# Performance work log

Hardware: AMD Instinct MI355X
Metric: run time of the kernel (lower is better)

Reference implementation:

```python
import jax, jax.numpy as jnp
import numpy as np

H = 128        # hidden_dim
NP = 512       # program nodes
NV = 50000     # voxel nodes
E = 800000     # cross edges (16 per voxel)
TAU = 1.0
SLOPE = 0.01   # LeakyReLU default negative slope


def setup_inputs() -> dict:
    key = jax.random.key(0)
    ks = jax.random.split(key, 12)
    s = 1.0 / np.sqrt(H)
    x = jax.random.normal(ks[0], (NP, H), dtype=jnp.float32)
    v = jax.random.normal(ks[1], (NV, H), dtype=jnp.float32)
    row0 = jax.random.randint(ks[2], (E,), 0, NP, dtype=jnp.int32)
    row1 = (jnp.arange(E, dtype=jnp.int32) % NV)  # every voxel gets E/NV edges
    cross_edge_index = jnp.stack([row0, row1])    # [2, E]
    W_program = jax.random.normal(ks[3], (H, H), dtype=jnp.float32) * s
    b_program = jnp.zeros((H,), dtype=jnp.float32)
    W_voxel = jax.random.normal(ks[4], (H, H), dtype=jnp.float32) * s
    b_voxel = jnp.zeros((H,), dtype=jnp.float32)
    W_m1 = jax.random.normal(ks[5], (H, H), dtype=jnp.float32) * s
    b_m1 = jnp.zeros((H,), dtype=jnp.float32)
    W_m2 = jax.random.normal(ks[6], (H, 1), dtype=jnp.float32) * s
    b_m2 = jnp.zeros((1,), dtype=jnp.float32)
    theta = jax.random.normal(ks[7], (H, 1), dtype=jnp.float32) * s  # xavier-like
    u = jax.random.uniform(ks[8], (E,), dtype=jnp.float32)
    gumbel_u = jnp.clip(u, 1e-7, 1.0 - 1e-7)  # avoid log(0)
    return {"x": x, "v": v, "cross_edge_index": cross_edge_index,
            "W_program": W_program, "b_program": b_program,
            "W_voxel": W_voxel, "b_voxel": b_voxel,
            "W_m1": W_m1, "b_m1": b_m1, "W_m2": W_m2, "b_m2": b_m2,
            "theta": theta, "gumbel_u": gumbel_u}


def reference(x, v, cross_edge_index, W_program, b_program, W_voxel, b_voxel,
              W_m1, b_m1, W_m2, b_m2, theta, gumbel_u):
    src = cross_edge_index[0]
    dst = cross_edge_index[1]
    x_sel = x[src]                      # [E, H] gather
    v_sel = v[dst]                      # [E, H] gather
    # mask = sigmoid(MLP(v)) : Linear -> LeakyReLU -> Linear(H,1)
    a = v @ W_m1 + b_m1
    a = jnp.where(a >= 0, a, SLOPE * a)
    mask = jax.nn.sigmoid(a @ W_m2 + b_m2)                  # [NV, 1]
    # attention logits: theta^T * tanh(Wp x_sel + Wv v_sel), summed over H
    t = jnp.tanh(x_sel @ W_program + b_program + v_sel @ W_voxel + b_voxel)
    e = jnp.sum(t * theta[:, 0], axis=-1)                   # [E]
    # Gumbel softmax: global softmax over all edges (dim=0 in torch on 1-D e)
    g = -jnp.log(-jnp.log(gumbel_u))
    y = jax.nn.softmax((e + g) / TAU)                       # [E]
    # per-voxel hard argmax (scatter_max), straight-through estimator
    seg_max = jax.ops.segment_max(y, dst, num_segments=NV)  # [NV]
    is_max = y == seg_max[dst]
    cand = jnp.where(is_max, jnp.arange(E), E)
    argmax = jax.ops.segment_min(cand, dst, num_segments=NV)  # [NV], first max per voxel
    y_hard_1 = jnp.zeros(E + 1, y.dtype).at[argmax].set(1.0)[:E]  # overflow slot for empty segments
    y_hard = jax.lax.stop_gradient(y_hard_1 - y) + y
    # scatter-sum of soft-attended program features back to voxels
    summed = jax.ops.segment_sum(x_sel * y[:, None], dst, num_segments=NV)  # [NV, H]
    v_out = v + mask * summed
    return (v_out, mask, y[:, None], y_hard[:, None])
```

## Files before the change

### kernel.cpp

```cpp
#include <hip/hip_runtime.h>

#define H     128
#define NP    512
#define NVOX  50000
#define NEDGE 800000
#define EPV   16
#define SLOPE 0.01f
#define GR    32
#define NBLK  1563
#define STRH  136
#define VSTR  132
#define C1    2.8853900817779268f
#define LOG2E 1.4426950408889634f
#define ABLK  3125

#define EXP2(x) __builtin_amdgcn_exp2f(x)
#define LOG2(x) __builtin_amdgcn_logf(x)
#define RCP(x)  __builtin_amdgcn_rcpf(x)

typedef _Float16 h16;
typedef __attribute__((ext_vector_type(4))) _Float16 h16x4;
typedef __attribute__((ext_vector_type(8))) _Float16 h16x8;
typedef __attribute__((ext_vector_type(4))) float    f32x4;

template <int CTRL>
__device__ __forceinline__ float dpp_add(float x) {
    union { float f; int i; } u, r;
    u.f = x;
    r.i = __builtin_amdgcn_update_dpp(0, u.i, CTRL, 0xf, 0xf, true);
    return x + r.f;
}

__global__ __launch_bounds__(256) void k_pre(const float* __restrict__ x,
                                             const float* __restrict__ Wp,
                                             const float* __restrict__ bp,
                                             const float* __restrict__ Wv,
                                             const float* __restrict__ Wm1,
                                             float* __restrict__ xpout,
                                             h16* __restrict__ WvThi,
                                             h16* __restrict__ WvTlo,
                                             h16* __restrict__ Wm1T) {
    __shared__ float part[H];
    int bid = blockIdx.x;
    int tid = threadIdx.x;
    if (bid < NP) {
        int row = bid;
        int col = tid & 127;
        int kh  = tid >> 7;
        int kbase = kh * 64;
        const float* xr = x + (size_t)row * H;
        float acc = 0.f;
#pragma unroll 8
        for (int k = 0; k < 64; ++k)
            acc = fmaf(xr[kbase + k], Wp[(size_t)(kbase + k) * H + col], acc);
        if (kh == 1) part[col] = acc;
        __syncthreads();
        if (kh == 0) xpout[(size_t)row * H + col] = (acc + part[col] + bp[col]) * C1;
    } else {
        int idx = (bid - NP) * 256 + tid;
        if (idx < 16384) {
            int k = idx >> 7, n = idx & 127;
            float w = Wv[idx];
            h16 hi = (h16)w;
            WvThi[n * H + k] = hi;
            WvTlo[n * H + k] = (h16)(w - (float)hi);
        } else {
            int j = idx - 16384;
            int k = j >> 7, n = j & 127;
            Wm1T[n * H + k] = (h16)Wm1[j];
        }
    }
}

__global__ __launch_bounds__(256, 4) void k_mainX(
    const float* __restrict__ v,   const float* __restrict__ x,
    const float* __restrict__ bv,  const float* __restrict__ bm1,
    const float* __restrict__ Wm2, const float* __restrict__ bm2,
    const h16* __restrict__ WvThi, const h16* __restrict__ WvTlo,
    const h16* __restrict__ Wm1T,
    const float* __restrict__ xp,  const int* __restrict__ cei,
    const float* __restrict__ theta, const float* __restrict__ gum,
    float* __restrict__ mask_out, float* __restrict__ pout,
    float* __restrict__ sump,     float* __restrict__ partial)
{
    __shared__ __align__(16) char ldsbuf[2 * GR * STRH * 2];
    h16*   vh = (h16*)ldsbuf;
    h16*   vl = vh + GR * STRH;
    float* vt = (float*)ldsbuf;
    __shared__ int   ceit[EPV * GR];
    __shared__ float gumt[EPV * GR];
    __shared__ float pmbuf[4][GR];
    __shared__ float psums[4];

    int tid  = threadIdx.x;
    int base = blockIdx.x * GR;

#pragma unroll
    for (int i = 0; i < 4; ++i) {
        int f  = i * 256 + tid;
        int r  = f >> 5, c4 = f & 31;
        int gr = base + r; if (gr >= NVOX) gr = NVOX - 1;
        float4 val = *(const float4*)&v[(size_t)gr * H + c4 * 4];
        h16x4 hi, lo;
        hi.x = (h16)val.x; lo.x = (h16)(val.x - (float)hi.x);
        hi.y = (h16)val.y; lo.y = (h16)(val.y - (float)hi.y);
        hi.z = (h16)val.z; lo.z = (h16)(val.z - (float)hi.z);
        hi.w = (h16)val.w; lo.w = (h16)(val.w - (float)hi.w);
        *(h16x4*)&vh[r * STRH + c4 * 4] = hi;
        *(h16x4*)&vl[r * STRH + c4 * 4] = lo;
    }
#pragma unroll
    for (int it = 0; it < 2; ++it) {
        int idx = it * 256 + tid;
        int t = idx >> 5, c = idx & 31;
        int vx = base + c; if (vx >= NVOX) vx = NVOX - 1;
        int e = vx + t * NVOX;
        ceit[idx] = cei[e];
        gumt[idx] = -LOG2E * RCP(LOG2(gum[e]));
    }
    __syncthreads();

    int wave = tid >> 6, lane = tid & 63;
    int m16 = lane & 15, quad = lane >> 4;
    int cb = wave * 32;

    f32x4 aV[2][2], aM[2][2];
#pragma unroll
    for (int rt = 0; rt < 2; ++rt)
#pragma unroll
        for (int ct = 0; ct < 2; ++ct) { aV[rt][ct] = (f32x4)0.f; aM[rt][ct] = (f32x4)0.f; }

#pragma unroll
    for (int kc = 0; kc < 4; ++kc) {
        int kofs = kc * 32 + quad * 8;
        h16x8 ah[2], al[2];
#pragma unroll
        for (int rt = 0; rt < 2; ++rt) {
            int row = rt * 16 + m16;
            ah[rt] = *(const h16x8*)&vh[row * STRH + kofs];
            al[rt] = *(const h16x8*)&vl[row * STRH + kofs];
        }
#pragma unroll
        for (int ct = 0; ct < 2; ++ct) {
            int n = cb + ct * 16 + m16;
            h16x8 bh = *(const h16x8*)&WvThi[n * H + kofs];
            h16x8 bl = *(const h16x8*)&WvTlo[n * H + kofs];
            h16x8 bm = *(const h16x8*)&Wm1T[n * H + kofs];
#pragma unroll
            for (int rt = 0; rt < 2; ++rt) {
                aV[rt][ct] = __builtin_amdgcn_mfma_f32_16x16x32_f16(ah[rt], bh, aV[rt][ct], 0, 0, 0);
                aV[rt][ct] = __builtin_amdgcn_mfma_f32_16x16x32_f16(al[rt], bh, aV[rt][ct], 0, 0, 0);
                aV[rt][ct] = __builtin_amdgcn_mfma_f32_16x16x32_f16(ah[rt], bl, aV[rt][ct], 0, 0, 0);
                aM[rt][ct] = __builtin_amdgcn_mfma_f32_16x16x32_f16(ah[rt], bm, aM[rt][ct], 0, 0, 0);
            }
        }
    }
    __syncthreads();

    float pml[2][4];
#pragma unroll
    for (int rt = 0; rt < 2; ++rt)
#pragma unroll
        for (int reg = 0; reg < 4; ++reg) pml[rt][reg] = 0.f;
#pragma unroll
    for (int ct = 0; ct < 2; ++ct) {
        int col = cb + ct * 16 + m16;
        float bvc = bv[col], bmc = bm1[col], w2c = Wm2[col];
#pragma unroll
        for (int rt = 0; rt < 2; ++rt)
#pragma unroll
            for (int reg = 0; reg < 4; ++reg) {
                int row = rt * 16 + quad * 4 + reg;
                vt[row * VSTR + col] = (aV[rt][ct][reg] + bvc) * C1;
                float m = aM[rt][ct][reg] + bmc;
                m = (m >= 0.f) ? m : SLOPE * m;
                pml[rt][reg] = fmaf(m, w2c, pml[rt][reg]);
            }
    }
#pragma unroll
    for (int rt = 0; rt < 2; ++rt)
#pragma unroll
        for (int reg = 0; reg < 4; ++reg) {
            pml[rt][reg] = dpp_add<0xB1>(pml[rt][reg]);
            pml[rt][reg] = dpp_add<0x4E>(pml[rt][reg]);
            pml[rt][reg] = dpp_add<0x141>(pml[rt][reg]);
            pml[rt][reg] = dpp_add<0x140>(pml[rt][reg]);
        }
    if (m16 == 0) {
#pragma unroll
        for (int rt = 0; rt < 2; ++rt)
#pragma unroll
            for (int reg = 0; reg < 4; ++reg)
                pmbuf[wave][rt * 16 + quad * 4 + reg] = pml[rt][reg];
    }
    __syncthreads();
    if (wave == 0 && lane < GR) {
        int gr = base + lane;
        if (gr < NVOX) {
            float s = pmbuf[0][lane] + pmbuf[1][lane] + pmbuf[2][lane]
                    + pmbuf[3][lane] + bm2[0];
            mask_out[gr] = RCP(1.f + EXP2(-s * LOG2E));
        }
    }

    int g = tid >> 3, lk = tid & 7;
    int vox = base + g;
    bool valid = vox < NVOX;
    float th2[16], thsum = 0.f;
#pragma unroll
    for (int i = 0; i < 4; ++i) {
        float4 t4 = *(const float4*)&theta[(lk + 8 * i) * 4];
        th2[i * 4 + 0] = -2.f * LOG2E * t4.x; th2[i * 4 + 1] = -2.f * LOG2E * t4.y;
        th2[i * 4 + 2] = -2.f * LOG2E * t4.z; th2[i * 4 + 3] = -2.f * LOG2E * t4.w;
        thsum += LOG2E * (t4.x + t4.y + t4.z + t4.w);
    }
    const float* vr = &vt[g * VSTR];
    float4 b0 = *(const float4*)&vr[(lk +  0) * 4];
    float4 b1 = *(const float4*)&vr[(lk +  8) * 4];
    float4 b2 = *(const float4*)&vr[(lk + 16) * 4];
    float4 b3 = *(const float4*)&vr[(lk + 24) * 4];

    float4 s0 = make_float4(0.f,0.f,0.f,0.f), s1 = s0, s2 = s0, s3 = s0;
    float psum = 0.f, pmax = -1.f;
    int   pidx = 0;

    int srcC = ceit[g];
    const float4* xr0 = (const float4*)(xp + (size_t)srcC * H);
    float4 a0 = xr0[lk], a1 = xr0[lk + 8], a2 = xr0[lk + 16], a3 = xr0[lk + 24];

    for (int t = 0; t < EPV; ++t) {
        float4 n0, n1, n2, n3;
        int srcN;
        if (t < EPV - 1) {
            srcN = ceit[(t + 1) * GR + g];
            const float4* xrN = (const float4*)(xp + (size_t)srcN * H);
            n0 = xrN[lk]; n1 = xrN[lk + 8]; n2 = xrN[lk + 16]; n3 = xrN[lk + 24];
        } else {
            srcN = srcC; n0 = a0; n1 = a1; n2 = a2; n3 = a3;
        }
        const float4* xo = (const float4*)(x + (size_t)srcC * H);
        float4 c0 = xo[lk], c1 = xo[lk + 8], c2 = xo[lk + 16], c3 = xo[lk + 24];
        float wvt = gumt[t * GR + g];

        float acc0 = thsum, acc1 = 0.f;
        acc0 = fmaf(th2[ 0], RCP(EXP2(a0.x + b0.x) + 1.f), acc0);
        acc1 = fmaf(th2[ 1], RCP(EXP2(a0.y + b0.y) + 1.f), acc1);
        acc0 = fmaf(th2[ 2], RCP(EXP2(a0.z + b0.z) + 1.f), acc0);
        acc1 = fmaf(th2[ 3], RCP(EXP2(a0.w + b0.w) + 1.f), acc1);
        acc0 = fmaf(th2[ 4], RCP(EXP2(a1.x + b1.x) + 1.f), acc0);
        acc1 = fmaf(th2[ 5], RCP(EXP2(a1.y + b1.y) + 1.f), acc1);
        acc0 = fmaf(th2[ 6], RCP(EXP2(a1.z + b1.z) + 1.f), acc0);
        acc1 = fmaf(th2[ 7], RCP(EXP2(a1.w + b1.w) + 1.f), acc1);
        acc0 = fmaf(th2[ 8], RCP(EXP2(a2.x + b2.x) + 1.f), acc0);
        acc1 = fmaf(th2[ 9], RCP(EXP2(a2.y + b2.y) + 1.f), acc1);
        acc0 = fmaf(th2[10], RCP(EXP2(a2.z + b2.z) + 1.f), acc0);
        acc1 = fmaf(th2[11], RCP(EXP2(a2.w + b2.w) + 1.f), acc1);
        acc0 = fmaf(th2[12], RCP(EXP2(a3.x + b3.x) + 1.f), acc0);
        acc1 = fmaf(th2[13], RCP(EXP2(a3.y + b3.y) + 1.f), acc1);
        acc0 = fmaf(th2[14], RCP(EXP2(a3.z + b3.z) + 1.f), acc0);
        acc1 = fmaf(th2[15], RCP(EXP2(a3.w + b3.w) + 1.f), acc1);
        float acc = acc0 + acc1;
        acc = dpp_add<0xB1>(acc);
        acc = dpp_add<0x4E>(acc);
        acc = dpp_add<0x141>(acc);
        float p = EXP2(acc) * wvt;
        if (p > pmax) { pmax = p; pidx = t; }
        if (valid) psum += p;
        if (lk == 0 && valid) pout[vox + t * NVOX] = p;
        s0.x = fmaf(p, c0.x, s0.x); s0.y = fmaf(p, c0.y, s0.y);
        s0.z = fmaf(p, c0.z, s0.z); s0.w = fmaf(p, c0.w, s0.w);
        s1.x = fmaf(p, c1.x, s1.x); s1.y = fmaf(p, c1.y, s1.y);
        s1.z = fmaf(p, c1.z, s1.z); s1.w = fmaf(p, c1.w, s1.w);
        s2.x = fmaf(p, c2.x, s2.x); s2.y = fmaf(p, c2.y, s2.y);
        s2.z = fmaf(p, c2.z, s2.z); s2.w = fmaf(p, c2.w, s2.w);
        s3.x = fmaf(p, c3.x, s3.x); s3.y = fmaf(p, c3.y, s3.y);
        s3.z = fmaf(p, c3.z, s3.z); s3.w = fmaf(p, c3.w, s3.w);
        a0 = n0; a1 = n1; a2 = n2; a3 = n3; srcC = srcN;
    }
    if (lk == 0 && valid) pout[vox + pidx * NVOX] = -pmax;
    if (valid) {
        float* sr = sump + (size_t)vox * H;
        *(float4*)&sr[(lk +  0) * 4] = s0;
        *(float4*)&sr[(lk +  8) * 4] = s1;
        *(float4*)&sr[(lk + 16) * 4] = s2;
        *(float4*)&sr[(lk + 24) * 4] = s3;
    }
    psum += __shfl_xor(psum, 8, 64);
    psum += __shfl_xor(psum, 16, 64);
    psum += __shfl_xor(psum, 32, 64);
    if (lane == 0) psums[wave] = psum;
    __syncthreads();
    if (tid == 0)
        partial[blockIdx.x] = psums[0] + psums[1] + psums[2] + psums[3];
}

__global__ __launch_bounds__(256) void k_out(const float* __restrict__ v,
                                             const float* __restrict__ maskp,
                                             const float* __restrict__ partial,
                                             float* __restrict__ vout,
                                             float* __restrict__ ybuf,
                                             float* __restrict__ yhard) {
    __shared__ float wsum[4];
    int tid = threadIdx.x;
    float s = 0.f;
    for (int i = tid; i < NBLK; i += 256) s += partial[i];
#pragma unroll
    for (int off = 32; off >= 1; off >>= 1) s += __shfl_xor(s, off, 64);
    if ((tid & 63) == 0) wsum[tid >> 6] = s;
    __syncthreads();
    float invS = RCP(wsum[0] + wsum[1] + wsum[2] + wsum[3]);

    int bid = blockIdx.x;
    if (bid < ABLK) {
#pragma unroll
        for (int r = 0; r < 2; ++r) {
            int i = (bid + r * ABLK) * 256 + tid;
            float4 sp = ((const float4*)vout)[i];
            float4 vv = ((const float4*)v)[i];
            float  m  = maskp[i >> 5] * invS;
            float4 o;
            o.x = fmaf(m, sp.x, vv.x); o.y = fmaf(m, sp.y, vv.y);
            o.z = fmaf(m, sp.z, vv.z); o.w = fmaf(m, sp.w, vv.w);
            ((float4*)vout)[i] = o;
        }
    } else {
        int e = (bid - ABLK) * 256 + tid;
        float pv = ybuf[e];
        ybuf[e]  = fabsf(pv) * invS;
        yhard[e] = (pv < 0.f) ? 1.f : 0.f;
    }
}

extern "C" void kernel_launch(void* const* d_in, const int* in_sizes, int n_in,
                              void* d_out, int out_size, void* d_ws, size_t ws_size,
                              hipStream_t stream) {
    (void)in_sizes; (void)n_in; (void)out_size; (void)ws_size;
    const float* x   = (const float*)d_in[0];
    const float* v   = (const float*)d_in[1];
    const int*   cei = (const int*)d_in[2];
    const float* Wp  = (const float*)d_in[3];
    const float* bp  = (const float*)d_in[4];
    const float* Wv  = (const float*)d_in[5];
    const float* bv  = (const float*)d_in[6];
    const float* Wm1 = (const float*)d_in[7];
    const float* bm1 = (const float*)d_in[8];
    const float* Wm2 = (const float*)d_in[9];
    const float* bm2 = (const float*)d_in[10];
    const float* th  = (const float*)d_in[11];
    const float* gum = (const float*)d_in[12];

    float* out   = (float*)d_out;
    float* vout  = out;
    float* maskp = out + (size_t)NVOX * H;
    float* ybuf  = maskp + NVOX;
    float* yhard = ybuf + NEDGE;
    float* xp    = yhard;
    h16*   WvThi = (h16*)(yhard + 65536);
    h16*   WvTlo = WvThi + 16384;
    h16*   Wm1T  = WvThi + 32768;
    float* partial = (float*)d_ws;

    k_pre<<<NP + 128, 256, 0, stream>>>(x, Wp, bp, Wv, Wm1, xp, WvThi, WvTlo, Wm1T);
    k_mainX<<<NBLK, 256, 0, stream>>>(v, x, bv, bm1, Wm2, bm2, WvThi, WvTlo, Wm1T,
                                      xp, cei, th, gum, maskp, ybuf, vout, partial);
    k_out<<<2 * ABLK, 256, 0, stream>>>(v, maskp, partial, vout, ybuf, yhard);
}
```

Measured before the change: 179.6 us.

## Fuse preprocessing into main kernel with ticket-based work and counter waits

Removes the separate precompute kernel. The first blocks to draw an atomic ticket compute the projected program features and the transposed fp16 weights, then publish completion through global counters, and every block spin-waits on those counters before using the results. Projected and raw program features are also interleaved into one 256-float row per node, so the edge loop's two gathers come from a single row instead of two arrays. This trades one kernel launch for a memset, atomics and spin-wait latency in the early blocks.

After: 623.9 us. +247.4%, slower.

```diff
diff --git a/kernel.cpp b/kernel.cpp
--- a/kernel.cpp
+++ b/kernel.cpp
@@ -13,6 +13,8 @@
 #define C1    2.8853900817779268f
 #define LOG2E 1.4426950408889634f
 #define ABLK  3125
+#define NPRE  704
+#define TXP   576
 
 #define EXP2(x) __builtin_amdgcn_exp2f(x)
 #define LOG2(x) __builtin_amdgcn_logf(x)
@@ -31,57 +33,27 @@
     return x + r.f;
 }
 
-__global__ __launch_bounds__(256) void k_pre(const float* __restrict__ x,
-                                             const float* __restrict__ Wp,
-                                             const float* __restrict__ bp,
-                                             const float* __restrict__ Wv,
-                                             const float* __restrict__ Wm1,
-                                             float* __restrict__ xpout,
-                                             h16* __restrict__ WvThi,
-                                             h16* __restrict__ WvTlo,
-                                             h16* __restrict__ Wm1T) {
-    __shared__ float part[H];
-    int bid = blockIdx.x;
-    int tid = threadIdx.x;
-    if (bid < NP) {
-        int row = bid;
-        int col = tid & 127;
-        int kh  = tid >> 7;
-        int kbase = kh * 64;
-        const float* xr = x + (size_t)row * H;
-        float acc = 0.f;
-#pragma unroll 8
-        for (int k = 0; k < 64; ++k)
-            acc = fmaf(xr[kbase + k], Wp[(size_t)(kbase + k) * H + col], acc);
-        if (kh == 1) part[col] = acc;
-        __syncthreads();
-        if (kh == 0) xpout[(size_t)row * H + col] = (acc + part[col] + bp[col]) * C1;
-    } else {
-        int idx = (bid - NP) * 256 + tid;
-        if (idx < 16384) {
-            int k = idx >> 7, n = idx & 127;
-            float w = Wv[idx];
-            h16 hi = (h16)w;
-            WvThi[n * H + k] = hi;
-            WvTlo[n * H + k] = (h16)(w - (float)hi);
-        } else {
-            int j = idx - 16384;
-            int k = j >> 7, n = j & 127;
-            Wm1T[n * H + k] = (h16)Wm1[j];
-        }
-    }
-}
-
-__global__ __launch_bounds__(256, 4) void k_mainX(
+__device__ __forceinline__ void waitctr(int* c, int target) {
+    if (threadIdx.x == 0)
+        while (__hip_atomic_load(c, __ATOMIC_RELAXED, __HIP_MEMORY_SCOPE_AGENT) < target)
+            __builtin_amdgcn_s_sleep(16);
+    __syncthreads();
+    __threadfence();
+}
+
+__global__ __launch_bounds__(256, 4) void k_fused(
     const float* __restrict__ v,   const float* __restrict__ x,
+    const float* __restrict__ Wp,  const float* __restrict__ bp,
+    const float* __restrict__ Wv,  const float* __restrict__ Wm1,
     const float* __restrict__ bv,  const float* __restrict__ bm1,
     const float* __restrict__ Wm2, const float* __restrict__ bm2,
-    const h16* __restrict__ WvThi, const h16* __restrict__ WvTlo,
-    const h16* __restrict__ Wm1T,
-    const float* __restrict__ xp,  const int* __restrict__ cei,
+    const int* __restrict__ cei,
     const float* __restrict__ theta, const float* __restrict__ gum,
-    float* __restrict__ mask_out, float* __restrict__ pout,
-    float* __restrict__ sump,     float* __restrict__ partial)
+    float* __restrict__ xc,        h16* __restrict__ WvThi,
+    h16* __restrict__ WvTlo,       h16* __restrict__ Wm1T,
+    float* __restrict__ mask_out,  float* __restrict__ pout,
+    float* __restrict__ sump,      float* __restrict__ partial,
+    int* __restrict__ ctrs)
 {
     __shared__ __align__(16) char ldsbuf[2 * GR * STRH * 2];
     h16*   vh = (h16*)ldsbuf;
@@ -91,9 +63,57 @@
     __shared__ float gumt[EPV * GR];
     __shared__ float pmbuf[4][GR];
     __shared__ float psums[4];
+    __shared__ int   tkt_s;
 
     int tid  = threadIdx.x;
     int base = blockIdx.x * GR;
+
+    if (tid == 0)
+        tkt_s = __hip_atomic_fetch_add(&ctrs[0], 1, __ATOMIC_RELAXED,
+                                       __HIP_MEMORY_SCOPE_AGENT);
+    __syncthreads();
+    int tkt = tkt_s;
+    if (tkt < NPRE) {
+        if (tkt < 512) {
+            float* part = (float*)ldsbuf;
+            int col = tid & 127, kh = tid >> 7, kbase = kh * 64;
+            const float* xr = x + (size_t)tkt * H;
+            float acc = 0.f;
+#pragma unroll 8
+            for (int k = 0; k < 64; ++k)
+                acc = fmaf(xr[kbase + k], Wp[(size_t)(kbase + k) * H + col], acc);
+            if (kh == 1) part[col] = acc;
+            __syncthreads();
+            if (kh == 0)
+                xc[(size_t)tkt * 256 + col] = (acc + part[col] + bp[col]) * C1;
+        } else if (tkt < 640) {
+            int idx = (tkt - 512) * 256 + tid;
+            if (idx < 16384) {
+                int k = idx >> 7, n = idx & 127;
+                float w = Wv[idx];
+                h16 hi = (h16)w;
+                WvThi[n * H + k] = hi;
+                WvTlo[n * H + k] = (h16)(w - (float)hi);
+            } else {
+                int j = idx - 16384;
+                int k = j >> 7, n = j & 127;
+                Wm1T[n * H + k] = (h16)Wm1[j];
+            }
+        } else {
+            int f4 = (tkt - 640) * 256 + tid;
+            int r = f4 >> 5, c4 = f4 & 31;
+            *(float4*)&xc[(size_t)r * 256 + 128 + c4 * 4] =
+                *(const float4*)&x[(size_t)r * H + c4 * 4];
+        }
+        __threadfence();
+        __syncthreads();
+        if (tid == 0) {
+            int* c = (tkt >= 512 && tkt < 640) ? &ctrs[1] : &ctrs[2];
+            __hip_atomic_fetch_add(c, 1, __ATOMIC_RELEASE,
+                                   __HIP_MEMORY_SCOPE_AGENT);
+        }
+        __syncthreads();
+    }
 
 #pragma unroll
     for (int i = 0; i < 4; ++i) {
@@ -120,6 +140,8 @@
     }
     __syncthreads();
 
+    waitctr(&ctrs[1], 128);
+
     int wave = tid >> 6, lane = tid & 63;
     int m16 = lane & 15, quad = lane >> 4;
     int cb = wave * 32;
@@ -203,6 +225,8 @@
         }
     }
 
+    waitctr(&ctrs[2], TXP);
+
     int g = tid >> 3, lk = tid & 7;
     int vox = base + g;
     bool valid = vox < NVOX;
@@ -224,22 +248,19 @@
     float psum = 0.f, pmax = -1.f;
     int   pidx = 0;
 
-    int srcC = ceit[g];
-    const float4* xr0 = (const float4*)(xp + (size_t)srcC * H);
-    float4 a0 = xr0[lk], a1 = xr0[lk + 8], a2 = xr0[lk + 16], a3 = xr0[lk + 24];
+    const float4* rC = (const float4*)(xc + (size_t)ceit[g] * 256);
+    float4 a0 = rC[lk], a1 = rC[lk + 8], a2 = rC[lk + 16], a3 = rC[lk + 24];
 
     for (int t = 0; t < EPV; ++t) {
+        const float4* rN;
         float4 n0, n1, n2, n3;
-        int srcN;
         if (t < EPV - 1) {
-            srcN = ceit[(t + 1) * GR + g];
-            const float4* xrN = (const float4*)(xp + (size_t)srcN * H);
-            n0 = xrN[lk]; n1 = xrN[lk + 8]; n2 = xrN[lk + 16]; n3 = xrN[lk + 24];
+            rN = (const float4*)(xc + (size_t)ceit[(t + 1) * GR + g] * 256);
+            n0 = rN[lk]; n1 = rN[lk + 8]; n2 = rN[lk + 16]; n3 = rN[lk + 24];
         } else {
-            srcN = srcC; n0 = a0; n1 = a1; n2 = a2; n3 = a3;
-        }
-        const float4* xo = (const float4*)(x + (size_t)srcC * H);
-        float4 c0 = xo[lk], c1 = xo[lk + 8], c2 = xo[lk + 16], c3 = xo[lk + 24];
+            rN = rC; n0 = a0; n1 = a1; n2 = a2; n3 = a3;
+        }
+        float4 c0 = rC[lk + 32], c1 = rC[lk + 40], c2 = rC[lk + 48], c3 = rC[lk + 56];
         float wvt = gumt[t * GR + g];
 
         float acc0 = thsum, acc1 = 0.f;
@@ -275,7 +296,7 @@
         s2.z = fmaf(p, c2.z, s2.z); s2.w = fmaf(p, c2.w, s2.w);
         s3.x = fmaf(p, c3.x, s3.x); s3.y = fmaf(p, c3.y, s3.y);
         s3.z = fmaf(p, c3.z, s3.z); s3.w = fmaf(p, c3.w, s3.w);
-        a0 = n0; a1 = n1; a2 = n2; a3 = n3; srcC = srcN;
+        a0 = n0; a1 = n1; a2 = n2; a3 = n3; rC = rN;
     }
     if (lk == 0 && valid) pout[vox + pidx * NVOX] = -pmax;
     if (valid) {
@@ -354,14 +375,16 @@
     float* maskp = out + (size_t)NVOX * H;
     float* ybuf  = maskp + NVOX;
     float* yhard = ybuf + NEDGE;
-    float* xp    = yhard;
-    h16*   WvThi = (h16*)(yhard + 65536);
+    float* xc    = yhard;
+    h16*   WvThi = (h16*)(yhard + 131072);
     h16*   WvTlo = WvThi + 16384;
     h16*   Wm1T  = WvThi + 32768;
     float* partial = (float*)d_ws;
-
-    k_pre<<<NP + 128, 256, 0, stream>>>(x, Wp, bp, Wv, Wm1, xp, WvThi, WvTlo, Wm1T);
-    k_mainX<<<NBLK, 256, 0, stream>>>(v, x, bv, bm1, Wm2, bm2, WvThi, WvTlo, Wm1T,
-                                      xp, cei, th, gum, maskp, ybuf, vout, partial);
+    int*   ctrs  = (int*)(partial + NBLK);
+
+    hipMemsetAsync(ctrs, 0, 16, stream);
+    k_fused<<<NBLK, 256, 0, stream>>>(v, x, Wp, bp, Wv, Wm1, bv, bm1, Wm2, bm2,
+                                      cei, th, gum, xc, WvThi, WvTlo, Wm1T,
+                                      maskp, ybuf, vout, partial, ctrs);
     k_out<<<2 * ABLK, 256, 0, stream>>>(v, maskp, partial, vout, ybuf, yhard);
 }
```
